# Kernel optimization log

Hardware: AMD Instinct MI355X
Metric: run time of the kernel (lower is better)

The kernel has to match this reference:

```python
import jax, jax.numpy as jnp
import numpy as np

N = 6144          # number_of_nodes
E = 196608        # random edges (self-loops appended in reference, as add_self_loops does)
L_GAT = 10        # GAT num_layers
NEG_SLOPE = 0.2   # GATConv leaky_relu slope


def setup_inputs() -> dict:
    key = jax.random.key(0)
    ks = jax.random.split(key, 27)
    g = lambda i, shape, s=0.3: jax.random.normal(ks[i], shape, jnp.float32) * s
    return {
        "x": jax.random.normal(ks[0], (N, 3), jnp.float32),
        "mask": jax.random.uniform(ks[1], (N,), dtype=jnp.float32),
        "edge_index": jax.random.randint(ks[2], (2, E), 0, N),
        # 10-layer GAT (heads=1): per-layer lin weight, att_src, att_dst, bias
        "gat_W": g(3, (L_GAT, 3, 3)), "gat_asrc": g(4, (L_GAT, 3)),
        "gat_adst": g(5, (L_GAT, 3)), "gat_b": g(6, (L_GAT, 3), 0.1),
        # nn.MultiheadAttention(embed_dim=3, num_heads=3)
        "mha_in_w": g(7, (9, 3)), "mha_in_b": g(8, (9,), 0.1),
        "mha_out_w": g(9, (3, 3)), "mha_out_b": g(10, (3,), 0.1),
        # TransformerConv(3, 3, heads=1)
        "tc_Wq": g(11, (3, 3)), "tc_bq": g(12, (3,), 0.1),
        "tc_Wk": g(13, (3, 3)), "tc_bk": g(14, (3,), 0.1),
        "tc_Wv": g(15, (3, 3)), "tc_bv": g(16, (3,), 0.1),
        "tc_Wskip": g(17, (3, 3)), "tc_bskip": g(18, (3,), 0.1),
        # actor MLP: Linear(3N,16) -> ReLU -> Linear(16,32) -> ReLU -> Linear(32,N)
        "mlp_W1": g(19, (3 * N, 16), 0.02), "mlp_b1": g(20, (16,), 0.1),
        "mlp_W2": g(21, (16, 32), 0.2), "mlp_b2": g(22, (32,), 0.1),
        "mlp_W3": g(23, (32, N), 0.2), "mlp_b3": jnp.zeros((N,), jnp.float32),
        # critic Linear(1,1)
        "critic_W": g(24, (1, 1)), "critic_b": g(25, (1,), 0.1),
    }


def _seg_softmax(e, seg, n):
    # numerically-stable softmax grouped by destination node
    m = jax.lax.stop_gradient(jax.ops.segment_max(e, seg, num_segments=n))
    w = jnp.exp(e - m[seg])
    z = jax.ops.segment_sum(w, seg, num_segments=n)
    return w / (z[seg] + 1e-16)


def reference(x, mask, edge_index, gat_W, gat_asrc, gat_adst, gat_b,
              mha_in_w, mha_in_b, mha_out_w, mha_out_b,
              tc_Wq, tc_bq, tc_Wk, tc_bk, tc_Wv, tc_bv, tc_Wskip, tc_bskip,
              mlp_W1, mlp_b1, mlp_W2, mlp_b2, mlp_W3, mlp_b3,
              critic_W, critic_b):
    n = x.shape[0]
    loops = jnp.arange(n)
    src = jnp.concatenate([edge_index[0], loops])  # add_self_loops
    dst = jnp.concatenate([edge_index[1], loops])

    # ---- 10-layer GAT (heads=1, ReLU between layers) ----
    h = x
    for l in range(L_GAT):
        xp = h @ gat_W[l]                                   # [N,3]
        e = jax.nn.leaky_relu(xp[src] @ gat_asrc[l] + xp[dst] @ gat_adst[l], NEG_SLOPE)
        alpha = _seg_softmax(e, dst, n)
        h_new = jax.ops.segment_sum(alpha[:, None] * xp[src], dst, num_segments=n) + gat_b[l]
        h = jax.nn.relu(h_new) if l < L_GAT - 1 else h_new

    # ---- MultiheadAttention(embed_dim=3, num_heads=3 => head_dim=1), history = [h] ----
    qkv = h @ mha_in_w.T + mha_in_b                         # [N,9]
    q, k, v = qkv[:, 0:3], qkv[:, 3:6], qkv[:, 6:9]
    scores = jnp.einsum('nh,mh->hnm', q, k)                 # head_dim=1 -> scale = 1
    attn = jax.nn.softmax(scores, axis=-1)                  # [3,N,N] -- dominant memory
    o = jnp.einsum('hnm,mh->nh', attn, v)                   # [N,3]
    h2 = o @ mha_out_w.T + mha_out_b

    # ---- TransformerConv(3, 3, heads=1) ----
    q2 = h2 @ tc_Wq + tc_bq
    k2 = h2 @ tc_Wk + tc_bk
    v2 = h2 @ tc_Wv + tc_bv
    logit = (q2[dst] * k2[src]).sum(-1) * (1.0 / np.sqrt(3.0))
    alpha2 = _seg_softmax(logit, dst, n)
    agg = jax.ops.segment_sum(alpha2[:, None] * v2[src], dst, num_segments=n)
    h3 = agg + h2 @ tc_Wskip + tc_bskip                     # root_weight skip

    # ---- actor MLP over flattened node features ----
    flat = h3.reshape(-1)                                   # [3N]
    a1 = jax.nn.relu(flat @ mlp_W1 + mlp_b1)
    a2 = jax.nn.relu(a1 @ mlp_W2 + mlp_b2)
    results = (a2 @ mlp_W3 + mlp_b3)[:, None]               # [N,1]

    new_results = results[:, 0] * mask
    value = jnp.mean(results @ critic_W + critic_b)
    return new_results, value
```

## Files before the change

### kernel.cpp

```cpp
#include <hip/hip_runtime.h>

#define N 6144
#define E 196608
#define EN (E + N)
#define LGAT 10

typedef unsigned int u32;

__device__ __forceinline__ u32 f2key(float f) {
    u32 u = __float_as_uint(f);
    return (u & 0x80000000u) ? ~u : (u | 0x80000000u);
}
__device__ __forceinline__ float key2f(u32 k) {
    u32 u = (k & 0x80000000u) ? (k & 0x7FFFFFFFu) : ~k;
    return __uint_as_float(u);
}

struct P {
    const float *x, *mask, *gat_W, *gat_asrc, *gat_adst, *gat_b;
    const float *in_w, *in_b, *out_w, *out_b;
    const float *Wq, *bq, *Wk, *bk, *Wv, *bv, *Wsk, *bsk;
    const float *W1, *b1, *W2, *b2, *W3, *b3, *cW, *cb;
    const int *src, *dst;
    float4 *nodeA, *nodeB;
    float *sdstA, *sdstB;
    float *qkv, *kvpack, *q2, *h2, *h3, *part;
    float4 *kv2;
    float *a1pre, *a2buf, *sumres;
    u32 *deg, *offs, *cursor, *kmaxk, *kmink;
    int *ssorted;
    float *out;
};

__global__ void k_hist(P p) {
    int e = blockIdx.x * 256 + threadIdx.x;
    if (e >= EN) return;
    int d = (e < E) ? p.dst[e] : (e - E);
    atomicAdd(&p.deg[d], 1u);
}

__global__ void k_scan(P p) {
    __shared__ u32 part[256];
    int t = threadIdx.x;
    if (t < 3) p.kmaxk[t] = 0u;
    else if (t < 6) p.kmink[t - 3] = 0xFFFFFFFFu;
    else if (t < 22) p.a1pre[t - 6] = 0.f;
    else if (t == 22) p.sumres[0] = 0.f;
    u32 loc[24];
    u32 sum = 0;
    #pragma unroll
    for (int i = 0; i < 24; ++i) { loc[i] = sum; sum += p.deg[t * 24 + i]; }
    part[t] = sum;
    __syncthreads();
    for (int o = 1; o < 256; o <<= 1) {
        u32 v = (t >= o) ? part[t - o] : 0u;
        __syncthreads();
        part[t] += v;
        __syncthreads();
    }
    u32 base = (t == 0) ? 0u : part[t - 1];
    #pragma unroll
    for (int i = 0; i < 24; ++i) {
        u32 off = base + loc[i];
        p.offs[t * 24 + i] = off;
        p.cursor[t * 24 + i] = off;
    }
    if (t == 255) p.offs[N] = part[255];
}

__global__ void k_scatter(P p) {
    int e = blockIdx.x * 256 + threadIdx.x;
    if (e >= EN) return;
    int s = (e < E) ? p.src[e] : (e - E);
    int d = (e < E) ? p.dst[e] : (e - E);
    u32 pos = atomicAdd(&p.cursor[d], 1u);
    p.ssorted[pos] = s;
}

__global__ void k_node0(P p) {
    int n = blockIdx.x * 256 + threadIdx.x;
    float h0 = p.x[n * 3 + 0], h1 = p.x[n * 3 + 1], h2 = p.x[n * 3 + 2];
    const float* W = p.gat_W;
    float xp0 = h0 * W[0] + h1 * W[3] + h2 * W[6];
    float xp1 = h0 * W[1] + h1 * W[4] + h2 * W[7];
    float xp2 = h0 * W[2] + h1 * W[5] + h2 * W[8];
    float ss = xp0 * p.gat_asrc[0] + xp1 * p.gat_asrc[1] + xp2 * p.gat_asrc[2];
    p.nodeA[n] = make_float4(xp0, xp1, xp2, ss);
    p.sdstA[n] = xp0 * p.gat_adst[0] + xp1 * p.gat_adst[1] + xp2 * p.gat_adst[2];
}

__global__ void k_gat_edge(P p, const float4* __restrict__ nin,
                           const float* __restrict__ sdin,
                           float4* __restrict__ nout, float* __restrict__ sdout,
                           int l) {
    int gid = blockIdx.x * 256 + threadIdx.x;
    int d = gid >> 5;
    int lane = gid & 31;
    u32 beg = p.offs[d], end = p.offs[d + 1];
    float sd = sdin[d];
    float mx = -1e30f;
    for (u32 i = beg + lane; i < end; i += 32) {
        float4 r = nin[p.ssorted[i]];
        float v = r.w + sd;
        v = (v >= 0.f) ? v : 0.2f * v;
        mx = fmaxf(mx, v);
    }
    #pragma unroll
    for (int o = 1; o < 32; o <<= 1) mx = fmaxf(mx, __shfl_xor(mx, o));
    float sz = 0.f, s0 = 0.f, s1 = 0.f, s2 = 0.f;
    for (u32 i = beg + lane; i < end; i += 32) {
        float4 r = nin[p.ssorted[i]];
        float v = r.w + sd;
        v = (v >= 0.f) ? v : 0.2f * v;
        float w = __expf(v - mx);
        sz += w;
        s0 += w * r.x; s1 += w * r.y; s2 += w * r.z;
    }
    #pragma unroll
    for (int o = 1; o < 32; o <<= 1) {
        sz += __shfl_xor(sz, o);
        s0 += __shfl_xor(s0, o);
        s1 += __shfl_xor(s1, o);
        s2 += __shfl_xor(s2, o);
    }
    if (lane == 0) {
        float z = sz + 1e-16f;
        float o0 = s0 / z + p.gat_b[l * 3 + 0];
        float o1 = s1 / z + p.gat_b[l * 3 + 1];
        float o2 = s2 / z + p.gat_b[l * 3 + 2];
        if (l < LGAT - 1) {
            o0 = fmaxf(o0, 0.f); o1 = fmaxf(o1, 0.f); o2 = fmaxf(o2, 0.f);
            const float* W = p.gat_W + (l + 1) * 9;
            float xp0 = o0 * W[0] + o1 * W[3] + o2 * W[6];
            float xp1 = o0 * W[1] + o1 * W[4] + o2 * W[7];
            float xp2 = o0 * W[2] + o1 * W[5] + o2 * W[8];
            const float* as = p.gat_asrc + (l + 1) * 3;
            const float* ad = p.gat_adst + (l + 1) * 3;
            float ss = xp0 * as[0] + xp1 * as[1] + xp2 * as[2];
            nout[d] = make_float4(xp0, xp1, xp2, ss);
            sdout[d] = xp0 * ad[0] + xp1 * ad[1] + xp2 * ad[2];
        } else {
            #pragma unroll
            for (int j = 0; j < 9; ++j) {
                float v = o0 * p.in_w[j * 3 + 0] + o1 * p.in_w[j * 3 + 1] +
                          o2 * p.in_w[j * 3 + 2] + p.in_b[j];
                p.qkv[d * 9 + j] = v;
            }
        }
    }
}

__global__ void k_kminmax(P p) {
    int n = blockIdx.x * 256 + threadIdx.x;
    float kk[3];
    #pragma unroll
    for (int hh = 0; hh < 3; ++hh) kk[hh] = p.qkv[n * 9 + 3 + hh];
    #pragma unroll
    for (int j = 0; j < 6; ++j) p.kvpack[n * 6 + j] = p.qkv[n * 9 + 3 + j];
    #pragma unroll
    for (int hh = 0; hh < 3; ++hh) {
        float mx = kk[hh], mn = kk[hh];
        #pragma unroll
        for (int o = 32; o; o >>= 1) {
            mx = fmaxf(mx, __shfl_xor(mx, o));
            mn = fminf(mn, __shfl_xor(mn, o));
        }
        if ((threadIdx.x & 63) == 0) {
            atomicMax(&p.kmaxk[hh], f2key(mx));
            atomicMin(&p.kmink[hh], f2key(mn));
        }
    }
}

#define MCH 192
__global__ void k_att_partial(P p) {
    int tid = threadIdx.x;
    int chunk = blockIdx.y;
    const float* __restrict__ kvp = p.kvpack + (size_t)chunk * MCH * 6;
    int n = blockIdx.x * 256 + tid;
    float q0 = p.qkv[n * 9 + 0], q1 = p.qkv[n * 9 + 1], q2 = p.qkv[n * 9 + 2];
    float kmx0 = key2f(p.kmaxk[0]), kmx1 = key2f(p.kmaxk[1]), kmx2 = key2f(p.kmaxk[2]);
    float kmn0 = key2f(p.kmink[0]), kmn1 = key2f(p.kmink[1]), kmn2 = key2f(p.kmink[2]);
    float M0 = (q0 >= 0.f) ? q0 * kmx0 : q0 * kmn0;
    float M1 = (q1 >= 0.f) ? q1 * kmx1 : q1 * kmn1;
    float M2 = (q2 >= 0.f) ? q2 * kmx2 : q2 * kmn2;
    float num0 = 0, den0 = 0, num1 = 0, den1 = 0, num2 = 0, den2 = 0;
    #pragma unroll 4
    for (int mm = 0; mm < MCH; ++mm) {
        float k0 = kvp[mm * 6 + 0], k1 = kvp[mm * 6 + 1], k2 = kvp[mm * 6 + 2];
        float v0 = kvp[mm * 6 + 3], v1 = kvp[mm * 6 + 4], v2 = kvp[mm * 6 + 5];
        float t0 = __expf(q0 * k0 - M0); den0 += t0; num0 += t0 * v0;
        float t1 = __expf(q1 * k1 - M1); den1 += t1; num1 += t1 * v1;
        float t2 = __expf(q2 * k2 - M2); den2 += t2; num2 += t2 * v2;
    }
    float* pp = p.part + (size_t)chunk * 6 * N + n;
    pp[0] = num0; pp[N] = den0; pp[2 * N] = num1;
    pp[3 * N] = den1; pp[4 * N] = num2; pp[5 * N] = den2;
}

__global__ void k_att_reduce(P p) {
    int n = blockIdx.x * 256 + threadIdx.x;
    float num[3] = {0.f, 0.f, 0.f}, den[3] = {0.f, 0.f, 0.f};
    for (int c = 0; c < 32; ++c) {
        const float* pp = p.part + (size_t)c * 6 * N + n;
        #pragma unroll
        for (int hh = 0; hh < 3; ++hh) {
            num[hh] += pp[hh * 2 * N];
            den[hh] += pp[(hh * 2 + 1) * N];
        }
    }
    float o[3];
    #pragma unroll
    for (int hh = 0; hh < 3; ++hh) o[hh] = num[hh] / den[hh];
    float h2v[3];
    #pragma unroll
    for (int c = 0; c < 3; ++c) {
        h2v[c] = p.out_b[c] + o[0] * p.out_w[c * 3 + 0] +
                 o[1] * p.out_w[c * 3 + 1] + o[2] * p.out_w[c * 3 + 2];
        p.h2[n * 3 + c] = h2v[c];
    }
    float q2v[3], k2v[3], v2v[3];
    #pragma unroll
    for (int c = 0; c < 3; ++c) {
        q2v[c] = p.bq[c] + h2v[0] * p.Wq[c] + h2v[1] * p.Wq[3 + c] + h2v[2] * p.Wq[6 + c];
        k2v[c] = p.bk[c] + h2v[0] * p.Wk[c] + h2v[1] * p.Wk[3 + c] + h2v[2] * p.Wk[6 + c];
        v2v[c] = p.bv[c] + h2v[0] * p.Wv[c] + h2v[1] * p.Wv[3 + c] + h2v[2] * p.Wv[6 + c];
        p.q2[n * 3 + c] = q2v[c];
    }
    p.kv2[n * 2 + 0] = make_float4(k2v[0], k2v[1], k2v[2], v2v[0]);
    p.kv2[n * 2 + 1] = make_float4(v2v[1], v2v[2], 0.f, 0.f);
}

__global__ void k_tc_edge(P p) {
    int gid = blockIdx.x * 256 + threadIdx.x;
    int d = gid >> 5;
    int lane = gid & 31;
    u32 beg = p.offs[d], end = p.offs[d + 1];
    float q0 = p.q2[d * 3 + 0], q1 = p.q2[d * 3 + 1], q2 = p.q2[d * 3 + 2];
    const float RS3 = 0.57735026919f;
    float mx = -1e30f;
    for (u32 i = beg + lane; i < end; i += 32) {
        float4 ka = p.kv2[p.ssorted[i] * 2];
        float lg = (q0 * ka.x + q1 * ka.y + q2 * ka.z) * RS3;
        mx = fmaxf(mx, lg);
    }
    #pragma unroll
    for (int o = 1; o < 32; o <<= 1) mx = fmaxf(mx, __shfl_xor(mx, o));
    float sz = 0.f, s0 = 0.f, s1 = 0.f, s2 = 0.f;
    for (u32 i = beg + lane; i < end; i += 32) {
        int s = p.ssorted[i];
        float4 ka = p.kv2[s * 2];
        float4 kb = p.kv2[s * 2 + 1];
        float lg = (q0 * ka.x + q1 * ka.y + q2 * ka.z) * RS3;
        float w = __expf(lg - mx);
        sz += w;
        s0 += w * ka.w; s1 += w * kb.x; s2 += w * kb.y;
    }
    #pragma unroll
    for (int o = 1; o < 32; o <<= 1) {
        sz += __shfl_xor(sz, o);
        s0 += __shfl_xor(s0, o);
        s1 += __shfl_xor(s1, o);
        s2 += __shfl_xor(s2, o);
    }
    if (lane == 0) {
        float z = sz + 1e-16f;
        float h0 = p.h2[d * 3 + 0], h1 = p.h2[d * 3 + 1], h2 = p.h2[d * 3 + 2];
        float agg[3] = {s0 / z, s1 / z, s2 / z};
        #pragma unroll
        for (int c = 0; c < 3; ++c) {
            p.h3[d * 3 + c] = agg[c] + p.bsk[c] +
                h0 * p.Wsk[c] + h1 * p.Wsk[3 + c] + h2 * p.Wsk[6 + c];
        }
    }
}

__global__ void k_mlp1(P p) {
    __shared__ float red[64];
    int t = blockIdx.x * 256 + threadIdx.x;
    int j = t & 15;
    int g = t >> 4;
    float acc = 0.f;
    #pragma unroll
    for (int k = 0; k < 16; ++k) {
        int r = g + k * 1152;
        acc += p.h3[r] * p.W1[r * 16 + j];
    }
    acc += __shfl_xor(acc, 16);
    acc += __shfl_xor(acc, 32);
    int tid = threadIdx.x;
    if ((tid & 63) < 16) red[(tid >> 6) * 16 + j] = acc;
    __syncthreads();
    if (tid < 16) {
        float s = red[tid] + red[16 + tid] + red[32 + tid] + red[48 + tid];
        atomicAdd(&p.a1pre[tid], s);
    }
}

__global__ void k_mlp2(P p) {
    __shared__ float a1[16];
    int t = threadIdx.x;
    if (t < 16) a1[t] = fmaxf(p.a1pre[t] + p.b1[t], 0.f);
    __syncthreads();
    if (t < 32) {
        float acc = p.b2[t];
        #pragma unroll
        for (int i = 0; i < 16; ++i) acc += a1[i] * p.W2[i * 32 + t];
        p.a2buf[t] = fmaxf(acc, 0.f);
    }
}

__global__ void k_mlp3(P p) {
    __shared__ float a2[32];
    if (threadIdx.x < 32) a2[threadIdx.x] = p.a2buf[threadIdx.x];
    __syncthreads();
    int n = blockIdx.x * 256 + threadIdx.x;
    float acc = p.b3[n];
    #pragma unroll
    for (int j = 0; j < 32; ++j) acc += a2[j] * p.W3[(size_t)j * N + n];
    p.out[n] = acc * p.mask[n];
    float s = acc;
    #pragma unroll
    for (int o = 32; o; o >>= 1) s += __shfl_xor(s, o);
    if ((threadIdx.x & 63) == 0) atomicAdd(p.sumres, s);
}

__global__ void k_value(P p) {
    p.out[N] = p.cW[0] * (p.sumres[0] / (float)N) + p.cb[0];
}

extern "C" void kernel_launch(void* const* d_in, const int* in_sizes, int n_in,
                              void* d_out, int out_size, void* d_ws, size_t ws_size,
                              hipStream_t stream) {
    P p;
    p.x      = (const float*)d_in[0];
    p.mask   = (const float*)d_in[1];
    const int* ei = (const int*)d_in[2];
    p.src = ei; p.dst = ei + E;
    p.gat_W  = (const float*)d_in[3];
    p.gat_asrc = (const float*)d_in[4];
    p.gat_adst = (const float*)d_in[5];
    p.gat_b  = (const float*)d_in[6];
    p.in_w   = (const float*)d_in[7];
    p.in_b   = (const float*)d_in[8];
    p.out_w  = (const float*)d_in[9];
    p.out_b  = (const float*)d_in[10];
    p.Wq = (const float*)d_in[11]; p.bq = (const float*)d_in[12];
    p.Wk = (const float*)d_in[13]; p.bk = (const float*)d_in[14];
    p.Wv = (const float*)d_in[15]; p.bv = (const float*)d_in[16];
    p.Wsk = (const float*)d_in[17]; p.bsk = (const float*)d_in[18];
    p.W1 = (const float*)d_in[19]; p.b1 = (const float*)d_in[20];
    p.W2 = (const float*)d_in[21]; p.b2 = (const float*)d_in[22];
    p.W3 = (const float*)d_in[23]; p.b3 = (const float*)d_in[24];
    p.cW = (const float*)d_in[25]; p.cb = (const float*)d_in[26];

    float* ws = (float*)d_ws;
    p.nodeA   = (float4*)(ws + 0);
    p.nodeB   = (float4*)(ws + 24576);
    p.sdstA   = ws + 49152;
    p.sdstB   = ws + 55296;
    p.qkv     = ws + 61440;
    p.kvpack  = ws + 116736;
    p.q2      = ws + 153600;
    p.kv2     = (float4*)(ws + 172032);
    p.h2      = ws + 221184;
    p.h3      = ws + 239616;
    p.part    = ws + 258048;
    p.a1pre   = ws + 1437696;
    p.a2buf   = ws + 1437712;
    p.sumres  = ws + 1437744;
    p.kmaxk   = (u32*)(ws + 1437748);
    p.kmink   = (u32*)(ws + 1437751);
    p.deg     = (u32*)(ws + 1437754);
    p.offs    = (u32*)(ws + 1443898);
    p.cursor  = (u32*)(ws + 1450043);
    p.ssorted = (int*)(ws + 1456187);
    p.out     = (float*)d_out;

    hipMemsetAsync(p.deg, 0, N * sizeof(u32), stream);
    k_hist<<<792, 256, 0, stream>>>(p);
    k_scan<<<1, 256, 0, stream>>>(p);
    k_scatter<<<792, 256, 0, stream>>>(p);
    k_node0<<<24, 256, 0, stream>>>(p);
    for (int l = 0; l < LGAT; ++l) {
        const float4* nin = (l & 1) ? p.nodeB : p.nodeA;
        const float*  sdin = (l & 1) ? p.sdstB : p.sdstA;
        float4* nout = (l & 1) ? p.nodeA : p.nodeB;
        float*  sdout = (l & 1) ? p.sdstA : p.sdstB;
        k_gat_edge<<<768, 256, 0, stream>>>(p, nin, sdin, nout, sdout, l);
    }
    k_kminmax<<<24, 256, 0, stream>>>(p);
    k_att_partial<<<dim3(24, 32), 256, 0, stream>>>(p);
    k_att_reduce<<<24, 256, 0, stream>>>(p);
    k_tc_edge<<<768, 256, 0, stream>>>(p);
    k_mlp1<<<72, 256, 0, stream>>>(p);
    k_mlp2<<<1, 64, 0, stream>>>(p);
    k_mlp3<<<24, 256, 0, stream>>>(p);
    k_value<<<1, 1, 0, stream>>>(p);
}
```

Measured before the change: 267.6 us.

## Fuse node0 into hist, use exp2 with prescaled logits, unroll edge loads, stage KV in LDS

Result: faster. 254.2 us (-5.0%).

```diff
diff --git a/kernel.cpp b/kernel.cpp
--- a/kernel.cpp
+++ b/kernel.cpp
@@ -4,6 +4,7 @@
 #define E 196608
 #define EN (E + N)
 #define LGAT 10
+#define LOG2E 1.4426950408889634f
 
 typedef unsigned int u32;
 
@@ -24,7 +25,8 @@
     const int *src, *dst;
     float4 *nodeA, *nodeB;
     float *sdstA, *sdstB;
-    float *qkv, *kvpack, *q2, *h2, *h3, *part;
+    float *q3, *q2, *h2, *h3, *part;
+    float4 *kvpack4;
     float4 *kv2;
     float *a1pre, *a2buf, *sumres;
     u32 *deg, *offs, *cursor, *kmaxk, *kmink;
@@ -34,6 +36,16 @@
 
 __global__ void k_hist(P p) {
     int e = blockIdx.x * 256 + threadIdx.x;
+    if (e < N) {
+        float h0 = p.x[e * 3 + 0], h1 = p.x[e * 3 + 1], h2 = p.x[e * 3 + 2];
+        const float* W = p.gat_W;
+        float xp0 = h0 * W[0] + h1 * W[3] + h2 * W[6];
+        float xp1 = h0 * W[1] + h1 * W[4] + h2 * W[7];
+        float xp2 = h0 * W[2] + h1 * W[5] + h2 * W[8];
+        float ss = LOG2E * (xp0 * p.gat_asrc[0] + xp1 * p.gat_asrc[1] + xp2 * p.gat_asrc[2]);
+        p.nodeA[e] = make_float4(xp0, xp1, xp2, ss);
+        p.sdstA[e] = LOG2E * (xp0 * p.gat_adst[0] + xp1 * p.gat_adst[1] + xp2 * p.gat_adst[2]);
+    }
     if (e >= EN) return;
     int d = (e < E) ? p.dst[e] : (e - E);
     atomicAdd(&p.deg[d], 1u);
@@ -77,18 +89,6 @@
     p.ssorted[pos] = s;
 }
 
-__global__ void k_node0(P p) {
-    int n = blockIdx.x * 256 + threadIdx.x;
-    float h0 = p.x[n * 3 + 0], h1 = p.x[n * 3 + 1], h2 = p.x[n * 3 + 2];
-    const float* W = p.gat_W;
-    float xp0 = h0 * W[0] + h1 * W[3] + h2 * W[6];
-    float xp1 = h0 * W[1] + h1 * W[4] + h2 * W[7];
-    float xp2 = h0 * W[2] + h1 * W[5] + h2 * W[8];
-    float ss = xp0 * p.gat_asrc[0] + xp1 * p.gat_asrc[1] + xp2 * p.gat_asrc[2];
-    p.nodeA[n] = make_float4(xp0, xp1, xp2, ss);
-    p.sdstA[n] = xp0 * p.gat_adst[0] + xp1 * p.gat_adst[1] + xp2 * p.gat_adst[2];
-}
-
 __global__ void k_gat_edge(P p, const float4* __restrict__ nin,
                            const float* __restrict__ sdin,
                            float4* __restrict__ nout, float* __restrict__ sdout,
@@ -98,23 +98,36 @@
     int lane = gid & 31;
     u32 beg = p.offs[d], end = p.offs[d + 1];
     float sd = sdin[d];
-    float mx = -1e30f;
-    for (u32 i = beg + lane; i < end; i += 32) {
+    u32 i0 = beg + lane, i1 = i0 + 32, i2 = i0 + 64, i3 = i0 + 96;
+    bool e0 = i0 < end, e1 = i1 < end, e2 = i2 < end, e3 = i3 < end;
+    int j0 = e0 ? p.ssorted[i0] : 0;
+    int j1 = e1 ? p.ssorted[i1] : 0;
+    int j2 = e2 ? p.ssorted[i2] : 0;
+    int j3 = e3 ? p.ssorted[i3] : 0;
+    float4 r0 = nin[j0], r1 = nin[j1], r2 = nin[j2], r3 = nin[j3];
+    float v0 = r0.w + sd; v0 = (v0 >= 0.f) ? v0 : 0.2f * v0; v0 = e0 ? v0 : -1e30f;
+    float v1 = r1.w + sd; v1 = (v1 >= 0.f) ? v1 : 0.2f * v1; v1 = e1 ? v1 : -1e30f;
+    float v2 = r2.w + sd; v2 = (v2 >= 0.f) ? v2 : 0.2f * v2; v2 = e2 ? v2 : -1e30f;
+    float v3 = r3.w + sd; v3 = (v3 >= 0.f) ? v3 : 0.2f * v3; v3 = e3 ? v3 : -1e30f;
+    float mx = fmaxf(fmaxf(v0, v1), fmaxf(v2, v3));
+    for (u32 i = i0 + 128; i < end; i += 32) {
         float4 r = nin[p.ssorted[i]];
-        float v = r.w + sd;
-        v = (v >= 0.f) ? v : 0.2f * v;
+        float v = r.w + sd; v = (v >= 0.f) ? v : 0.2f * v;
         mx = fmaxf(mx, v);
     }
     #pragma unroll
     for (int o = 1; o < 32; o <<= 1) mx = fmaxf(mx, __shfl_xor(mx, o));
-    float sz = 0.f, s0 = 0.f, s1 = 0.f, s2 = 0.f;
-    for (u32 i = beg + lane; i < end; i += 32) {
+    float w0 = exp2f(v0 - mx), w1 = exp2f(v1 - mx),
+          w2 = exp2f(v2 - mx), w3 = exp2f(v3 - mx);
+    float sz = w0 + w1 + w2 + w3;
+    float s0 = w0 * r0.x + w1 * r1.x + w2 * r2.x + w3 * r3.x;
+    float s1 = w0 * r0.y + w1 * r1.y + w2 * r2.y + w3 * r3.y;
+    float s2 = w0 * r0.z + w1 * r1.z + w2 * r2.z + w3 * r3.z;
+    for (u32 i = i0 + 128; i < end; i += 32) {
         float4 r = nin[p.ssorted[i]];
-        float v = r.w + sd;
-        v = (v >= 0.f) ? v : 0.2f * v;
-        float w = __expf(v - mx);
-        sz += w;
-        s0 += w * r.x; s1 += w * r.y; s2 += w * r.z;
+        float v = r.w + sd; v = (v >= 0.f) ? v : 0.2f * v;
+        float w = exp2f(v - mx);
+        sz += w; s0 += w * r.x; s1 += w * r.y; s2 += w * r.z;
     }
     #pragma unroll
     for (int o = 1; o < 32; o <<= 1) {
@@ -136,27 +149,26 @@
             float xp2 = o0 * W[2] + o1 * W[5] + o2 * W[8];
             const float* as = p.gat_asrc + (l + 1) * 3;
             const float* ad = p.gat_adst + (l + 1) * 3;
-            float ss = xp0 * as[0] + xp1 * as[1] + xp2 * as[2];
+            float ss = LOG2E * (xp0 * as[0] + xp1 * as[1] + xp2 * as[2]);
             nout[d] = make_float4(xp0, xp1, xp2, ss);
-            sdout[d] = xp0 * ad[0] + xp1 * ad[1] + xp2 * ad[2];
+            sdout[d] = LOG2E * (xp0 * ad[0] + xp1 * ad[1] + xp2 * ad[2]);
         } else {
+            float pr[9];
             #pragma unroll
-            for (int j = 0; j < 9; ++j) {
-                float v = o0 * p.in_w[j * 3 + 0] + o1 * p.in_w[j * 3 + 1] +
-                          o2 * p.in_w[j * 3 + 2] + p.in_b[j];
-                p.qkv[d * 9 + j] = v;
-            }
+            for (int j = 0; j < 9; ++j)
+                pr[j] = o0 * p.in_w[j * 3 + 0] + o1 * p.in_w[j * 3 + 1] +
+                        o2 * p.in_w[j * 3 + 2] + p.in_b[j];
+            p.q3[d * 3 + 0] = pr[0]; p.q3[d * 3 + 1] = pr[1]; p.q3[d * 3 + 2] = pr[2];
+            p.kvpack4[d * 2 + 0] = make_float4(pr[3], pr[4], pr[5], pr[6]);
+            p.kvpack4[d * 2 + 1] = make_float4(pr[7], pr[8], 0.f, 0.f);
         }
     }
 }
 
 __global__ void k_kminmax(P p) {
     int n = blockIdx.x * 256 + threadIdx.x;
-    float kk[3];
-    #pragma unroll
-    for (int hh = 0; hh < 3; ++hh) kk[hh] = p.qkv[n * 9 + 3 + hh];
-    #pragma unroll
-    for (int j = 0; j < 6; ++j) p.kvpack[n * 6 + j] = p.qkv[n * 9 + 3 + j];
+    float4 a = p.kvpack4[n * 2];
+    float kk[3] = {a.x, a.y, a.z};
     #pragma unroll
     for (int hh = 0; hh < 3; ++hh) {
         float mx = kk[hh], mn = kk[hh];
@@ -174,24 +186,27 @@
 
 #define MCH 192
 __global__ void k_att_partial(P p) {
+    __shared__ float4 kv4[MCH * 2];
     int tid = threadIdx.x;
     int chunk = blockIdx.y;
-    const float* __restrict__ kvp = p.kvpack + (size_t)chunk * MCH * 6;
+    int mbase = chunk * MCH;
+    for (int i = tid; i < MCH * 2; i += 256) kv4[i] = p.kvpack4[mbase * 2 + i];
+    __syncthreads();
     int n = blockIdx.x * 256 + tid;
-    float q0 = p.qkv[n * 9 + 0], q1 = p.qkv[n * 9 + 1], q2 = p.qkv[n * 9 + 2];
+    float q0 = p.q3[n * 3 + 0], q1 = p.q3[n * 3 + 1], q2 = p.q3[n * 3 + 2];
     float kmx0 = key2f(p.kmaxk[0]), kmx1 = key2f(p.kmaxk[1]), kmx2 = key2f(p.kmaxk[2]);
     float kmn0 = key2f(p.kmink[0]), kmn1 = key2f(p.kmink[1]), kmn2 = key2f(p.kmink[2]);
-    float M0 = (q0 >= 0.f) ? q0 * kmx0 : q0 * kmn0;
-    float M1 = (q1 >= 0.f) ? q1 * kmx1 : q1 * kmn1;
-    float M2 = (q2 >= 0.f) ? q2 * kmx2 : q2 * kmn2;
+    float q0s = q0 * LOG2E, q1s = q1 * LOG2E, q2s = q2 * LOG2E;
+    float nM0 = -((q0 >= 0.f) ? q0s * kmx0 : q0s * kmn0);
+    float nM1 = -((q1 >= 0.f) ? q1s * kmx1 : q1s * kmn1);
+    float nM2 = -((q2 >= 0.f) ? q2s * kmx2 : q2s * kmn2);
     float num0 = 0, den0 = 0, num1 = 0, den1 = 0, num2 = 0, den2 = 0;
     #pragma unroll 4
     for (int mm = 0; mm < MCH; ++mm) {
-        float k0 = kvp[mm * 6 + 0], k1 = kvp[mm * 6 + 1], k2 = kvp[mm * 6 + 2];
-        float v0 = kvp[mm * 6 + 3], v1 = kvp[mm * 6 + 4], v2 = kvp[mm * 6 + 5];
-        float t0 = __expf(q0 * k0 - M0); den0 += t0; num0 += t0 * v0;
-        float t1 = __expf(q1 * k1 - M1); den1 += t1; num1 += t1 * v1;
-        float t2 = __expf(q2 * k2 - M2); den2 += t2; num2 += t2 * v2;
+        float4 a = kv4[mm * 2], b = kv4[mm * 2 + 1];
+        float t0 = exp2f(fmaf(q0s, a.x, nM0)); den0 += t0; num0 = fmaf(t0, a.w, num0);
+        float t1 = exp2f(fmaf(q1s, a.y, nM1)); den1 += t1; num1 = fmaf(t1, b.x, num1);
+        float t2 = exp2f(fmaf(q2s, a.z, nM2)); den2 += t2; num2 = fmaf(t2, b.y, num2);
     }
     float* pp = p.part + (size_t)chunk * 6 * N + n;
     pp[0] = num0; pp[N] = den0; pp[2 * N] = num1;
@@ -237,24 +252,33 @@
     int lane = gid & 31;
     u32 beg = p.offs[d], end = p.offs[d + 1];
     float q0 = p.q2[d * 3 + 0], q1 = p.q2[d * 3 + 1], q2 = p.q2[d * 3 + 2];
-    const float RS3 = 0.57735026919f;
-    float mx = -1e30f;
-    for (u32 i = beg + lane; i < end; i += 32) {
+    const float RS3L = 0.57735026919f * LOG2E;
+    u32 i0 = beg + lane, i1 = i0 + 32;
+    bool e0 = i0 < end, e1 = i1 < end;
+    int j0 = e0 ? p.ssorted[i0] : 0;
+    int j1 = e1 ? p.ssorted[i1] : 0;
+    float4 ka0 = p.kv2[j0 * 2], kb0 = p.kv2[j0 * 2 + 1];
+    float4 ka1 = p.kv2[j1 * 2], kb1 = p.kv2[j1 * 2 + 1];
+    float g0 = (q0 * ka0.x + q1 * ka0.y + q2 * ka0.z) * RS3L; g0 = e0 ? g0 : -1e30f;
+    float g1 = (q0 * ka1.x + q1 * ka1.y + q2 * ka1.z) * RS3L; g1 = e1 ? g1 : -1e30f;
+    float mx = fmaxf(g0, g1);
+    for (u32 i = i0 + 64; i < end; i += 32) {
         float4 ka = p.kv2[p.ssorted[i] * 2];
-        float lg = (q0 * ka.x + q1 * ka.y + q2 * ka.z) * RS3;
-        mx = fmaxf(mx, lg);
+        mx = fmaxf(mx, (q0 * ka.x + q1 * ka.y + q2 * ka.z) * RS3L);
     }
     #pragma unroll
     for (int o = 1; o < 32; o <<= 1) mx = fmaxf(mx, __shfl_xor(mx, o));
-    float sz = 0.f, s0 = 0.f, s1 = 0.f, s2 = 0.f;
-    for (u32 i = beg + lane; i < end; i += 32) {
+    float w0 = exp2f(g0 - mx), w1 = exp2f(g1 - mx);
+    float sz = w0 + w1;
+    float s0 = w0 * ka0.w + w1 * ka1.w;
+    float s1 = w0 * kb0.x + w1 * kb1.x;
+    float s2 = w0 * kb0.y + w1 * kb1.y;
+    for (u32 i = i0 + 64; i < end; i += 32) {
         int s = p.ssorted[i];
-        float4 ka = p.kv2[s * 2];
-        float4 kb = p.kv2[s * 2 + 1];
-        float lg = (q0 * ka.x + q1 * ka.y + q2 * ka.z) * RS3;
-        float w = __expf(lg - mx);
-        sz += w;
-        s0 += w * ka.w; s1 += w * kb.x; s2 += w * kb.y;
+        float4 ka = p.kv2[s * 2], kb = p.kv2[s * 2 + 1];
+        float g = (q0 * ka.x + q1 * ka.y + q2 * ka.z) * RS3L;
+        float w = exp2f(g - mx);
+        sz += w; s0 += w * ka.w; s1 += w * kb.x; s2 += w * kb.y;
     }
     #pragma unroll
     for (int o = 1; o < 32; o <<= 1) {
@@ -359,29 +383,28 @@
     p.nodeB   = (float4*)(ws + 24576);
     p.sdstA   = ws + 49152;
     p.sdstB   = ws + 55296;
-    p.qkv     = ws + 61440;
-    p.kvpack  = ws + 116736;
-    p.q2      = ws + 153600;
-    p.kv2     = (float4*)(ws + 172032);
-    p.h2      = ws + 221184;
-    p.h3      = ws + 239616;
-    p.part    = ws + 258048;
-    p.a1pre   = ws + 1437696;
-    p.a2buf   = ws + 1437712;
-    p.sumres  = ws + 1437744;
-    p.kmaxk   = (u32*)(ws + 1437748);
-    p.kmink   = (u32*)(ws + 1437751);
-    p.deg     = (u32*)(ws + 1437754);
-    p.offs    = (u32*)(ws + 1443898);
-    p.cursor  = (u32*)(ws + 1450043);
-    p.ssorted = (int*)(ws + 1456187);
+    p.q3      = ws + 61440;
+    p.kvpack4 = (float4*)(ws + 79872);
+    p.q2      = ws + 129024;
+    p.kv2     = (float4*)(ws + 147456);
+    p.h2      = ws + 196608;
+    p.h3      = ws + 215040;
+    p.part    = ws + 233472;
+    p.a1pre   = ws + 1413120;
+    p.a2buf   = ws + 1413136;
+    p.sumres  = ws + 1413168;
+    p.kmaxk   = (u32*)(ws + 1413172);
+    p.kmink   = (u32*)(ws + 1413175);
+    p.deg     = (u32*)(ws + 1413178);
+    p.offs    = (u32*)(ws + 1419322);
+    p.cursor  = (u32*)(ws + 1425467);
+    p.ssorted = (int*)(ws + 1431611);
     p.out     = (float*)d_out;
 
     hipMemsetAsync(p.deg, 0, N * sizeof(u32), stream);
     k_hist<<<792, 256, 0, stream>>>(p);
     k_scan<<<1, 256, 0, stream>>>(p);
     k_scatter<<<792, 256, 0, stream>>>(p);
-    k_node0<<<24, 256, 0, stream>>>(p);
     for (int l = 0; l < LGAT; ++l) {
         const float4* nin = (l & 1) ? p.nodeB : p.nodeA;
         const float*  sdin = (l & 1) ? p.sdstB : p.sdstA;
```
